# Kernel tuning notes

Hardware: AMD Instinct MI355X
Metric: run time of the kernel (lower is better)

## Reference

```python
import jax, jax.numpy as jnp
import numpy as np

N, E, R = 50000, 500000, 3
IN, HID, OUT = 128, 128, 128
NEG_SLOPE = 0.2


def setup_inputs() -> dict:
    key = jax.random.key(0)
    ks = jax.random.split(key, 16)
    g = lambda i, shape: jax.random.normal(ks[i], shape, jnp.float32) * 0.1
    return {
        "x": jax.random.normal(ks[0], (N, IN), jnp.float32),
        "edge_index": jax.random.randint(ks[1], (2, E), 0, N, jnp.int32),
        "edge_type": jax.random.randint(ks[2], (E,), 0, R, jnp.int32),
        "edge_attr": jax.random.normal(ks[3], (E, 1), jnp.float32),
        # conv1 params (RGATConv: per-relation weight, q/k/e attention vectors, edge lin, bias)
        "w1": g(4, (R, IN, HID)), "q1": g(5, (HID, 1)), "k1": g(6, (HID, 1)),
        "le1": g(7, (1, HID)), "e1": g(8, (HID, 1)), "b1": jnp.zeros((HID,), jnp.float32),
        # conv2 params
        "w2": g(9, (R, HID, OUT)), "q2": g(10, (OUT, 1)), "k2": g(11, (OUT, 1)),
        "le2": g(12, (1, OUT)), "e2": g(13, (OUT, 1)), "b2": jnp.zeros((OUT,), jnp.float32),
    }


def _rgat_conv(x, src, dst, edge_type, edge_attr, w, q, k, le, e, b):
    """PyG RGATConv: heads=1, dim=1, additive-self-attention, across-relation softmax."""
    n = x.shape[0]
    # Per-relation linear at node level (equiv. to per-edge bmm with w[edge_type])
    xw = jnp.einsum('ni,rio->rno', x, w)            # [R, N, C]
    x_j = xw[edge_type, src]                          # [E, C] transformed source feats
    x_i = xw[edge_type, dst]                          # [E, C] transformed target feats
    # additive attention logits: q(x_i) + k(x_j) + e(lin_edge(edge_attr))
    alpha = x_i @ q + x_j @ k + (edge_attr @ le) @ e  # [E, 1]
    alpha = jax.nn.leaky_relu(alpha, negative_slope=NEG_SLOPE)
    # across-relation softmax over incoming edges of each target node
    amax = jax.ops.segment_max(alpha, dst, num_segments=n)
    amax = jnp.where(jnp.isfinite(amax), amax, 0.0)   # empty segments -> 0
    ex = jnp.exp(alpha - amax[dst])
    denom = jax.ops.segment_sum(ex, dst, num_segments=n)
    alpha = ex / (denom[dst] + 1e-16)
    # weighted scatter-add aggregation, then bias (concat=True, heads=1)
    out = jax.ops.segment_sum(alpha * x_j, dst, num_segments=n)  # [N, C]
    return out + b


def reference(x, edge_index, edge_type, edge_attr,
              w1, q1, k1, le1, e1, b1,
              w2, q2, k2, le2, e2, b2):
    src, dst = edge_index[0], edge_index[1]
    h = jax.nn.relu(_rgat_conv(x, src, dst, edge_type, edge_attr, w1, q1, k1, le1, e1, b1))
    return _rgat_conv(h, src, dst, edge_type, edge_attr, w2, q2, k2, le2, e2, b2)
```

## Files before the change

kernel.cpp:

```cpp
#include <hip/hip_runtime.h>
#include <hip/hip_bf16.h>
#include <math.h>

typedef __bf16 bf16x8 __attribute__((ext_vector_type(8)));
typedef float f32x4 __attribute__((ext_vector_type(4)));

#define CDIM 128

__global__ void sentinel_kernel(float* outf) {
  if (threadIdx.x == 0) outf[0] = 12345.0f;
}

__global__ __launch_bounds__(256) void prep_hist_kernel(
    const float* __restrict__ w1, const float* __restrict__ w2,
    __hip_bfloat16* __restrict__ wt,
    const float* __restrict__ le1, const float* __restrict__ e1,
    const float* __restrict__ le2, const float* __restrict__ e2,
    float* __restrict__ outc, const int* __restrict__ dstv,
    int* __restrict__ deg, int perW, int E) {
  const int b = blockIdx.x;
  const int tid = threadIdx.x;
  if (b < 48) {
    int t = b * 256 + tid;
    if (t >= perW * 2) return;
    const float* w = (t < perW) ? w1 : w2;
    int tt = (t < perW) ? t : t - perW;
    int r = tt >> 11;
    int rem = tt & 2047;
    int kb = rem >> 7;
    int o = rem & 127;
    const float* wr = w + ((size_t)r << 14);
    union { __hip_bfloat16 h[8]; int4 v; } u;
#pragma unroll
    for (int j = 0; j < 8; ++j)
      u.h[j] = __float2bfloat16(wr[(size_t)(kb * 8 + j) * CDIM + o]);
    *reinterpret_cast<int4*>(wt + (size_t)t * 8) = u.v;
  } else if (b == 48) {
    if (tid < 64) {
      float v1 = le1[tid] * e1[tid] + le1[tid + 64] * e1[tid + 64];
      float v2 = le2[tid] * e2[tid] + le2[tid + 64] * e2[tid + 64];
#pragma unroll
      for (int off = 32; off > 0; off >>= 1) {
        v1 += __shfl_xor(v1, off, 64);
        v2 += __shfl_xor(v2, off, 64);
      }
      if (tid == 0) { outc[0] = v1; outc[1] = v2; }
    }
  } else {
    int e0 = (b - 49) * 1024 + tid * 4;
    if (e0 + 3 < E) {
      int4 d4 = *reinterpret_cast<const int4*>(&dstv[e0]);
      atomicAdd(&deg[d4.x], 1);
      atomicAdd(&deg[d4.y], 1);
      atomicAdd(&deg[d4.z], 1);
      atomicAdd(&deg[d4.w], 1);
    } else {
      for (int t = 0; t < 4; ++t) {
        int e = e0 + t;
        if (e < E) atomicAdd(&deg[dstv[e]], 1);
      }
    }
  }
}


__global__ __launch_bounds__(256) void scan1_kernel(const int* __restrict__ deg,
                                                    int* __restrict__ rowptr,
                                                    int* __restrict__ partials, int n) {
  __shared__ int sh[256];
  int t = threadIdx.x;
  int base = blockIdx.x * 1024;
  int idx = base + t * 4;
  int v[4]; int s = 0;
#pragma unroll
  for (int j = 0; j < 4; ++j) { v[j] = (idx + j < n) ? deg[idx + j] : 0; s += v[j]; }
  sh[t] = s;
  __syncthreads();
  for (int off = 1; off < 256; off <<= 1) {
    int x = (t >= off) ? sh[t - off] : 0;
    __syncthreads();
    sh[t] += x;
    __syncthreads();
  }
  int excl = sh[t] - s;
  if (t == 255) partials[blockIdx.x] = sh[255];
  int run = excl;
#pragma unroll
  for (int j = 0; j < 4; ++j) {
    if (idx + j < n) rowptr[idx + j] = run;
    run += v[j];
  }
}

__global__ __launch_bounds__(256) void scan3_kernel(int* __restrict__ rowptr,
                                                    int* __restrict__ cursor,
                                                    const int* __restrict__ partials,
                                                    int nb, int n, int E) {
  __shared__ int spfx[64];
  int t = threadIdx.x;
  if (t < 64) {
    int pv = (t < nb) ? partials[t] : 0;
    int v = pv;
#pragma unroll
    for (int off = 1; off < 64; off <<= 1) {
      int u = __shfl_up(v, off, 64);
      if (t >= off) v += u;
    }
    spfx[t] = v - pv;
  }
  __syncthreads();
  int i = blockIdx.x * 256 + t;
  if (i < n) {
    int v = rowptr[i] + spfx[i >> 10];
    rowptr[i] = v;
    cursor[i] = v;
  } else if (i == n) {
    rowptr[n] = E;
  }
}

template <int BF16IN>
__device__ __forceinline__ void gemm_body128(
    int tileb, const float* __restrict__ xf, const __hip_bfloat16* __restrict__ xb,
    const __hip_bfloat16* __restrict__ wt,
    const float* __restrict__ qv, const float* __restrict__ kv,
    __hip_bfloat16* __restrict__ xwout, float* __restrict__ sq,
    float* __restrict__ sk, int n, __hip_bfloat16* wlds, float* qls, float* kls) {
  const int base = tileb * 128;
  const int tid = threadIdx.x;
  const int wave = tid >> 6, lane = tid & 63;
  const int quad = lane >> 4, c16 = lane & 15;

  if (tid < 128) qls[tid] = qv[tid];
  else kls[tid - 128] = kv[tid - 128];

  bf16x8 zf;
#pragma unroll
  for (int j = 0; j < 8; ++j) zf[j] = (__bf16)0.0f;

  bf16x8 af[2][4];
#pragma unroll
  for (int h = 0; h < 2; ++h) {
    int m = base + wave * 32 + h * 16 + c16;
#pragma unroll
    for (int ks = 0; ks < 4; ++ks) {
      if (m < n) {
        if (BF16IN) {
          af[h][ks] = *reinterpret_cast<const bf16x8*>(
              xb + (size_t)m * CDIM + ks * 32 + quad * 8);
        } else {
          const float* xp = xf + (size_t)m * CDIM + ks * 32 + quad * 8;
          f32x4 x0 = *reinterpret_cast<const f32x4*>(xp);
          f32x4 x1 = *reinterpret_cast<const f32x4*>(xp + 4);
          bf16x8 a;
#pragma unroll
          for (int j = 0; j < 4; ++j) { a[j] = (__bf16)x0[j]; a[4 + j] = (__bf16)x1[j]; }
          af[h][ks] = a;
        }
      } else {
        af[h][ks] = zf;
      }
    }
  }

  for (int r = 0; r < 3; ++r) {
    if (r) __syncthreads();
    {
      const int4* src = reinterpret_cast<const int4*>(wt + ((size_t)r << 14));
      int4* dst = reinterpret_cast<int4*>(wlds);
#pragma unroll
      for (int i = 0; i < 8; ++i) dst[tid + i * 256] = src[tid + i * 256];
    }
    __syncthreads();

    f32x4 acc[2][8];
#pragma unroll
    for (int h = 0; h < 2; ++h)
#pragma unroll
      for (int ot = 0; ot < 8; ++ot) acc[h][ot] = (f32x4){0.f, 0.f, 0.f, 0.f};

#pragma unroll
    for (int ks = 0; ks < 4; ++ks) {
#pragma unroll
      for (int ot = 0; ot < 8; ++ot) {
        bf16x8 b = *reinterpret_cast<const bf16x8*>(
            &wlds[(((ks * 4 + quad) * 128) + ot * 16 + c16) * 8]);
        acc[0][ot] = __builtin_amdgcn_mfma_f32_16x16x32_bf16(b, af[0][ks], acc[0][ot], 0, 0, 0);
        acc[1][ot] = __builtin_amdgcn_mfma_f32_16x16x32_bf16(b, af[1][ks], acc[1][ot], 0, 0, 0);
      }
    }

#pragma unroll
    for (int h = 0; h < 2; ++h) {
      const int grow = base + wave * 32 + h * 16 + c16;
      const bool ok = grow < n;
      __hip_bfloat16* rp = xwout + (((size_t)r * n + grow) << 7) + quad * 4;
      float s_q = 0.f, s_k = 0.f;
#pragma unroll
      for (int ot = 0; ot < 8; ++ot) {
        f32x4 a = acc[h][ot];
        f32x4 q4 = *reinterpret_cast<const f32x4*>(&qls[ot * 16 + quad * 4]);
        f32x4 k4 = *reinterpret_cast<const f32x4*>(&kls[ot * 16 + quad * 4]);
        s_q += a[0] * q4[0] + a[1] * q4[1] + a[2] * q4[2] + a[3] * q4[3];
        s_k += a[0] * k4[0] + a[1] * k4[1] + a[2] * k4[2] + a[3] * k4[3];
        if (ok) {
          union { __hip_bfloat16 b4[4]; uint2 u; } pk;
#pragma unroll
          for (int t = 0; t < 4; ++t) pk.b4[t] = __float2bfloat16(a[t]);
          *reinterpret_cast<uint2*>(rp + ot * 16) = pk.u;
        }
      }
      s_q += __shfl_xor(s_q, 16, 64);
      s_q += __shfl_xor(s_q, 32, 64);
      s_k += __shfl_xor(s_k, 16, 64);
      s_k += __shfl_xor(s_k, 32, 64);
      if (quad == 0 && ok) {
        sq[(size_t)r * n + grow] = s_q;
        sk[(size_t)r * n + grow] = s_k;
      }
    }
  }
}

__global__ __launch_bounds__(256) void gemm_scatter_kernel(
    const float* __restrict__ xin, const __hip_bfloat16* __restrict__ wt,
    const float* __restrict__ qv, const float* __restrict__ kv,
    __hip_bfloat16* __restrict__ xwout, float* __restrict__ sq, float* __restrict__ sk,
    const int* __restrict__ srcv, const int* __restrict__ dstv,
    const int* __restrict__ etype, const float* __restrict__ eattr,
    int* __restrict__ cursor, int2* __restrict__ kattr,
    int NT, int n, int E) {
  __shared__ __hip_bfloat16 wlds[16 * 128 * 8];
  __shared__ float qls[128], kls[128];
  const int b = blockIdx.x;
  if (b < NT) {
    gemm_body128<0>(b, xin, nullptr, wt, qv, kv, xwout, sq, sk, n, wlds, qls, kls);
  } else {
    int e0 = (b - NT) * 1024 + threadIdx.x * 4;
    if (e0 + 3 < E) {
      int4 s4 = *reinterpret_cast<const int4*>(&srcv[e0]);
      int4 d4 = *reinterpret_cast<const int4*>(&dstv[e0]);
      int4 t4 = *reinterpret_cast<const int4*>(&etype[e0]);
      float4 a4 = *reinterpret_cast<const float4*>(&eattr[e0]);
      int p0 = atomicAdd(&cursor[d4.x], 1);
      kattr[p0] = make_int2(t4.x * n + s4.x, __float_as_int(a4.x));
      int p1 = atomicAdd(&cursor[d4.y], 1);
      kattr[p1] = make_int2(t4.y * n + s4.y, __float_as_int(a4.y));
      int p2 = atomicAdd(&cursor[d4.z], 1);
      kattr[p2] = make_int2(t4.z * n + s4.z, __float_as_int(a4.z));
      int p3 = atomicAdd(&cursor[d4.w], 1);
      kattr[p3] = make_int2(t4.w * n + s4.w, __float_as_int(a4.w));
    } else {
      for (int t = 0; t < 4; ++t) {
        int e = e0 + t;
        if (e < E) {
          int p = atomicAdd(&cursor[dstv[e]], 1);
          kattr[p] = make_int2(etype[e] * n + srcv[e], __float_as_int(eattr[e]));
        }
      }
    }
  }
}

__global__ __launch_bounds__(256) void gemm_xw_bf16_kernel(
    const __hip_bfloat16* __restrict__ xin, const __hip_bfloat16* __restrict__ wt,
    const float* __restrict__ qv, const float* __restrict__ kv,
    __hip_bfloat16* __restrict__ xwout, float* __restrict__ sq, float* __restrict__ sk,
    int n) {
  __shared__ __hip_bfloat16 wlds[16 * 128 * 8];
  __shared__ float qls[128], kls[128];
  gemm_body128<1>(blockIdx.x, nullptr, xin, wt, qv, kv, xwout, sq, sk, n,
                  wlds, qls, kls);
}

template <int OUTBF16>
__global__ __launch_bounds__(256) void aggregate_kernel(
    const int* __restrict__ rowptr, const int2* __restrict__ kattr,
    const float* __restrict__ sq, const float* __restrict__ sk,
    const __hip_bfloat16* __restrict__ xw, const float* __restrict__ bias,
    const float* __restrict__ cscal, float* __restrict__ outf,
    __hip_bfloat16* __restrict__ outb, int n) {
  const int wave = threadIdx.x >> 6, lane = threadIdx.x & 63;
  const int g = lane >> 4;
  const int sub = lane & 15;
  const int node = blockIdx.x * 16 + wave * 4 + g;
  if (node >= n) return;
  const float c = cscal[0];
  const int n2 = n * 2;

  const int start = rowptr[node];
  const int deg = rowptr[node + 1] - start;
  const float s0 = sq[node], s1 = sq[n + node], s2 = sq[n2 + node];

  float acc[8];
#pragma unroll
  for (int t = 0; t < 8; ++t) acc[t] = 0.f;
  float den = 0.f;

  for (int j0 = 0; j0 < deg; j0 += 4) {
    int2 ka[4];
#pragma unroll
    for (int t = 0; t < 4; ++t) {
      int idx = j0 + t;
      ka[t] = kattr[start + (idx < deg ? idx : 0)];
    }
    float w[4];
    bf16x8 f[4];
#pragma unroll
    for (int t = 0; t < 4; ++t) {
      int kk = ka[t].x;
      float sv = (kk >= n2) ? s2 : ((kk >= n) ? s1 : s0);
      float l = sv + sk[kk] + c * __int_as_float(ka[t].y);
      l = l > 0.f ? l : 0.2f * l;
      w[t] = (j0 + t < deg) ? __expf(l) : 0.f;
      f[t] = *reinterpret_cast<const bf16x8*>(xw + ((size_t)kk << 7) + sub * 8);
    }
#pragma unroll
    for (int t = 0; t < 8; ++t)
      acc[t] += w[0] * (float)f[0][t] + w[1] * (float)f[1][t] +
                w[2] * (float)f[2][t] + w[3] * (float)f[3][t];
    den += (w[0] + w[1]) + (w[2] + w[3]);
  }

  float inv = 1.0f / (den + 1e-16f);
  f32x4 b0 = *reinterpret_cast<const f32x4*>(bias + sub * 8);
  f32x4 b1 = *reinterpret_cast<const f32x4*>(bias + sub * 8 + 4);
  f32x4 o0, o1;
#pragma unroll
  for (int t = 0; t < 4; ++t) {
    o0[t] = acc[t] * inv + b0[t];
    o1[t] = acc[4 + t] * inv + b1[t];
  }
  if (OUTBF16) {
    union { __hip_bfloat16 h[8]; int4 v; } pk;
#pragma unroll
    for (int t = 0; t < 4; ++t) {
      pk.h[t] = __float2bfloat16(fmaxf(o0[t], 0.f));
      pk.h[4 + t] = __float2bfloat16(fmaxf(o1[t], 0.f));
    }
    *reinterpret_cast<int4*>(outb + (size_t)node * CDIM + sub * 8) = pk.v;
  } else {
    float* op = outf + (size_t)node * CDIM + sub * 8;
    *reinterpret_cast<f32x4*>(op) = o0;
    *reinterpret_cast<f32x4*>(op + 4) = o1;
  }
}


extern "C" void kernel_launch(void* const* d_in, const int* in_sizes, int n_in,
                              void* d_out, int out_size, void* d_ws, size_t ws_size,
                              hipStream_t stream) {
  const float* x     = (const float*)d_in[0];
  const int*   eidx  = (const int*)d_in[1];
  const int*   etype = (const int*)d_in[2];
  const float* eattr = (const float*)d_in[3];
  const float* w1  = (const float*)d_in[4];
  const float* q1  = (const float*)d_in[5];
  const float* k1  = (const float*)d_in[6];
  const float* le1 = (const float*)d_in[7];
  const float* e1  = (const float*)d_in[8];
  const float* b1  = (const float*)d_in[9];
  const float* w2  = (const float*)d_in[10];
  const float* q2  = (const float*)d_in[11];
  const float* k2  = (const float*)d_in[12];
  const float* le2 = (const float*)d_in[13];
  const float* e2  = (const float*)d_in[14];
  const float* b2  = (const float*)d_in[15];

  const int N = in_sizes[0] / CDIM;
  const int E = in_sizes[2];
  const int R = in_sizes[4] / (CDIM * CDIM);
  const int* srcv = eidx;
  const int* dstv = eidx + E;

  char* p = (char*)d_ws;
  auto alloc = [&](size_t bytes) -> void* {
    void* q = (void*)p;
    p += (bytes + 255) & ~(size_t)255;
    return q;
  };
  float* sq       = (float*)alloc((size_t)R * N * 4);
  float* sk       = (float*)alloc((size_t)R * N * 4);
  int*   deg      = (int*)alloc((size_t)N * 4);
  int*   rowptr   = (int*)alloc((size_t)(N + 1) * 4);
  int*   cursor   = (int*)alloc((size_t)N * 4);
  int*   partials = (int*)alloc(4096);
  int2*  kattr    = (int2*)alloc((size_t)E * 8);
  __hip_bfloat16* wt = (__hip_bfloat16*)alloc((size_t)2 * R * CDIM * CDIM * 2);
  float* cscal    = (float*)alloc(256);
  __hip_bfloat16* xw = (__hip_bfloat16*)alloc((size_t)R * N * CDIM * 2);
  __hip_bfloat16* hb = (__hip_bfloat16*)alloc((size_t)N * CDIM * 2);

  size_t needed = (size_t)(p - (char*)d_ws);
  if (needed > ws_size) {
    sentinel_kernel<<<1, 64, 0, stream>>>((float*)d_out);
    return;
  }

  float* outp = (float*)d_out;

  const int eg4 = (E + 1023) / 1024;
  const int nb = (N + 1023) / 1024;
  const int NT = (N + 127) / 128;
  const int nodes16 = (N + 15) / 16;
  const int perW = R * 2048;

  hipMemsetAsync(deg, 0, (size_t)N * 4, stream);

  prep_hist_kernel<<<49 + eg4, 256, 0, stream>>>(w1, w2, wt, le1, e1, le2, e2,
                                                 cscal, dstv, deg, perW, E);

  scan1_kernel<<<nb, 256, 0, stream>>>(deg, rowptr, partials, N);
  scan3_kernel<<<(N + 1 + 255) / 256, 256, 0, stream>>>(rowptr, cursor, partials, nb, N, E);

  gemm_scatter_kernel<<<NT + eg4, 256, 0, stream>>>(x, wt, q1, k1, xw, sq, sk,
                                                    srcv, dstv, etype, eattr,
                                                    cursor, kattr, NT, N, E);

  aggregate_kernel<1><<<nodes16, 256, 0, stream>>>(rowptr, kattr, sq, sk, xw, b1,
                                                   cscal + 0, nullptr, hb, N);

  gemm_xw_bf16_kernel<<<NT, 256, 0, stream>>>(hb, wt + (size_t)R * CDIM * CDIM,
                                              q2, k2, xw, sq, sk, N);

  aggregate_kernel<0><<<nodes16, 256, 0, stream>>>(rowptr, kattr, sq, sk, xw, b2,
                                                   cscal + 1, outp, nullptr, N);
}
```

Baseline: 239.8 us.

## Fuse layer-1 aggregation with layer-2 relation GEMM via shared-memory hidden tile

Merges the first aggregation kernel with the second layer's per-relation GEMM. Each block aggregates 64 nodes into a bf16 tile in shared memory and then runs MFMA directly on that tile, so the hidden activation never goes through global memory and one launch is removed. Layer-2 xw, sq and sk now go to separate buffers because other blocks may still be reading layer-1 xw. The trade-offs are that weights are read from global or L2 instead of being staged in LDS, the GEMM tile shrinks to 64 rows, and the workspace grows.

```diff
diff --git a/kernel.cpp b/kernel.cpp
--- a/kernel.cpp
+++ b/kernel.cpp
@@ -119,9 +119,8 @@
   }
 }
 
-template <int BF16IN>
 __device__ __forceinline__ void gemm_body128(
-    int tileb, const float* __restrict__ xf, const __hip_bfloat16* __restrict__ xb,
+    int tileb, const float* __restrict__ xf,
     const __hip_bfloat16* __restrict__ wt,
     const float* __restrict__ qv, const float* __restrict__ kv,
     __hip_bfloat16* __restrict__ xwout, float* __restrict__ sq,
@@ -145,18 +144,13 @@
 #pragma unroll
     for (int ks = 0; ks < 4; ++ks) {
       if (m < n) {
-        if (BF16IN) {
-          af[h][ks] = *reinterpret_cast<const bf16x8*>(
-              xb + (size_t)m * CDIM + ks * 32 + quad * 8);
-        } else {
-          const float* xp = xf + (size_t)m * CDIM + ks * 32 + quad * 8;
-          f32x4 x0 = *reinterpret_cast<const f32x4*>(xp);
-          f32x4 x1 = *reinterpret_cast<const f32x4*>(xp + 4);
-          bf16x8 a;
-#pragma unroll
-          for (int j = 0; j < 4; ++j) { a[j] = (__bf16)x0[j]; a[4 + j] = (__bf16)x1[j]; }
-          af[h][ks] = a;
-        }
+        const float* xp = xf + (size_t)m * CDIM + ks * 32 + quad * 8;
+        f32x4 x0 = *reinterpret_cast<const f32x4*>(xp);
+        f32x4 x1 = *reinterpret_cast<const f32x4*>(xp + 4);
+        bf16x8 a;
+#pragma unroll
+        for (int j = 0; j < 4; ++j) { a[j] = (__bf16)x0[j]; a[4 + j] = (__bf16)x1[j]; }
+        af[h][ks] = a;
       } else {
         af[h][ks] = zf;
       }
@@ -234,7 +228,7 @@
   __shared__ float qls[128], kls[128];
   const int b = blockIdx.x;
   if (b < NT) {
-    gemm_body128<0>(b, xin, nullptr, wt, qv, kv, xwout, sq, sk, n, wlds, qls, kls);
+    gemm_body128(b, xin, wt, qv, kv, xwout, sq, sk, n, wlds, qls, kls);
   } else {
     int e0 = (b - NT) * 1024 + threadIdx.x * 4;
     if (e0 + 3 < E) {
@@ -262,24 +256,138 @@
   }
 }
 
-__global__ __launch_bounds__(256) void gemm_xw_bf16_kernel(
-    const __hip_bfloat16* __restrict__ xin, const __hip_bfloat16* __restrict__ wt,
+__global__ __launch_bounds__(256) void agg_gemm_kernel(
+    const int* __restrict__ rowptr, const int2* __restrict__ kattr,
+    const float* __restrict__ sq1, const float* __restrict__ sk1,
+    const __hip_bfloat16* __restrict__ xw1, const float* __restrict__ bias1,
+    const float* __restrict__ cscal,
+    const __hip_bfloat16* __restrict__ wt2,
     const float* __restrict__ qv, const float* __restrict__ kv,
-    __hip_bfloat16* __restrict__ xwout, float* __restrict__ sq, float* __restrict__ sk,
-    int n) {
-  __shared__ __hip_bfloat16 wlds[16 * 128 * 8];
+    __hip_bfloat16* __restrict__ xw2, float* __restrict__ sq2,
+    float* __restrict__ sk2, int n) {
+  __shared__ __hip_bfloat16 hb[64][144];
   __shared__ float qls[128], kls[128];
-  gemm_body128<1>(blockIdx.x, nullptr, xin, wt, qv, kv, xwout, sq, sk, n,
-                  wlds, qls, kls);
-}
-
-template <int OUTBF16>
+  const int tid = threadIdx.x;
+  const int nodeBase = blockIdx.x * 64;
+  const int grp = tid >> 4, sub = tid & 15;
+  const float c = cscal[0];
+  const int n2 = n * 2;
+
+  if (tid < 128) qls[tid] = qv[tid];
+  else kls[tid - 128] = kv[tid - 128];
+
+#pragma unroll
+  for (int i = 0; i < 4; ++i) {
+    const int lrow = grp * 4 + i;
+    const int node = nodeBase + lrow;
+    if (node < n) {
+      const int start = rowptr[node];
+      const int deg = rowptr[node + 1] - start;
+      const float s0 = sq1[node], s1 = sq1[n + node], s2 = sq1[n2 + node];
+
+      float acc[8];
+#pragma unroll
+      for (int t = 0; t < 8; ++t) acc[t] = 0.f;
+      float den = 0.f;
+
+      for (int j0 = 0; j0 < deg; j0 += 4) {
+        int2 ka[4];
+#pragma unroll
+        for (int t = 0; t < 4; ++t) {
+          int idx = j0 + t;
+          ka[t] = kattr[start + (idx < deg ? idx : 0)];
+        }
+        float w[4];
+        bf16x8 f[4];
+#pragma unroll
+        for (int t = 0; t < 4; ++t) {
+          int kk = ka[t].x;
+          float sv = (kk >= n2) ? s2 : ((kk >= n) ? s1 : s0);
+          float l = sv + sk1[kk] + c * __int_as_float(ka[t].y);
+          l = l > 0.f ? l : 0.2f * l;
+          w[t] = (j0 + t < deg) ? __expf(l) : 0.f;
+          f[t] = *reinterpret_cast<const bf16x8*>(xw1 + ((size_t)kk << 7) + sub * 8);
+        }
+#pragma unroll
+        for (int t = 0; t < 8; ++t)
+          acc[t] += w[0] * (float)f[0][t] + w[1] * (float)f[1][t] +
+                    w[2] * (float)f[2][t] + w[3] * (float)f[3][t];
+        den += (w[0] + w[1]) + (w[2] + w[3]);
+      }
+
+      float inv = 1.0f / (den + 1e-16f);
+      f32x4 b0 = *reinterpret_cast<const f32x4*>(bias1 + sub * 8);
+      f32x4 b1 = *reinterpret_cast<const f32x4*>(bias1 + sub * 8 + 4);
+      union { __hip_bfloat16 h[8]; int4 v; } pk;
+#pragma unroll
+      for (int t = 0; t < 4; ++t) {
+        pk.h[t] = __float2bfloat16(fmaxf(acc[t] * inv + b0[t], 0.f));
+        pk.h[4 + t] = __float2bfloat16(fmaxf(acc[4 + t] * inv + b1[t], 0.f));
+      }
+      *reinterpret_cast<int4*>(&hb[lrow][sub * 8]) = pk.v;
+    }
+  }
+  __syncthreads();
+
+  const int wave = tid >> 6, lane = tid & 63;
+  const int quad = lane >> 4, c16 = lane & 15;
+  const int lrow = wave * 16 + c16;
+  const int m = nodeBase + lrow;
+  const bool ok = m < n;
+
+  bf16x8 af[4];
+#pragma unroll
+  for (int ks = 0; ks < 4; ++ks)
+    af[ks] = *reinterpret_cast<const bf16x8*>(&hb[lrow][ks * 32 + quad * 8]);
+
+  for (int r = 0; r < 3; ++r) {
+    const __hip_bfloat16* wr = wt2 + ((size_t)r << 14);
+    f32x4 acc[8];
+#pragma unroll
+    for (int ot = 0; ot < 8; ++ot) acc[ot] = (f32x4){0.f, 0.f, 0.f, 0.f};
+
+#pragma unroll
+    for (int ks = 0; ks < 4; ++ks) {
+#pragma unroll
+      for (int ot = 0; ot < 8; ++ot) {
+        bf16x8 b = *reinterpret_cast<const bf16x8*>(
+            wr + (size_t)((((ks * 4 + quad) * 128) + ot * 16 + c16) * 8));
+        acc[ot] = __builtin_amdgcn_mfma_f32_16x16x32_bf16(b, af[ks], acc[ot], 0, 0, 0);
+      }
+    }
+
+    __hip_bfloat16* rp = xw2 + (((size_t)r * n + m) << 7) + quad * 4;
+    float s_q = 0.f, s_k = 0.f;
+#pragma unroll
+    for (int ot = 0; ot < 8; ++ot) {
+      f32x4 a = acc[ot];
+      f32x4 q4 = *reinterpret_cast<const f32x4*>(&qls[ot * 16 + quad * 4]);
+      f32x4 k4 = *reinterpret_cast<const f32x4*>(&kls[ot * 16 + quad * 4]);
+      s_q += a[0] * q4[0] + a[1] * q4[1] + a[2] * q4[2] + a[3] * q4[3];
+      s_k += a[0] * k4[0] + a[1] * k4[1] + a[2] * k4[2] + a[3] * k4[3];
+      if (ok) {
+        union { __hip_bfloat16 b4[4]; uint2 u; } pk;
+#pragma unroll
+        for (int t = 0; t < 4; ++t) pk.b4[t] = __float2bfloat16(a[t]);
+        *reinterpret_cast<uint2*>(rp + ot * 16) = pk.u;
+      }
+    }
+    s_q += __shfl_xor(s_q, 16, 64);
+    s_q += __shfl_xor(s_q, 32, 64);
+    s_k += __shfl_xor(s_k, 16, 64);
+    s_k += __shfl_xor(s_k, 32, 64);
+    if (quad == 0 && ok) {
+      sq2[(size_t)r * n + m] = s_q;
+      sk2[(size_t)r * n + m] = s_k;
+    }
+  }
+}
+
 __global__ __launch_bounds__(256) void aggregate_kernel(
     const int* __restrict__ rowptr, const int2* __restrict__ kattr,
     const float* __restrict__ sq, const float* __restrict__ sk,
     const __hip_bfloat16* __restrict__ xw, const float* __restrict__ bias,
-    const float* __restrict__ cscal, float* __restrict__ outf,
-    __hip_bfloat16* __restrict__ outb, int n) {
+    const float* __restrict__ cscal, float* __restrict__ out, int n) {
   const int wave = threadIdx.x >> 6, lane = threadIdx.x & 63;
   const int g = lane >> 4;
   const int sub = lane & 15;
@@ -331,19 +439,9 @@
     o0[t] = acc[t] * inv + b0[t];
     o1[t] = acc[4 + t] * inv + b1[t];
   }
-  if (OUTBF16) {
-    union { __hip_bfloat16 h[8]; int4 v; } pk;
-#pragma unroll
-    for (int t = 0; t < 4; ++t) {
-      pk.h[t] = __float2bfloat16(fmaxf(o0[t], 0.f));
-      pk.h[4 + t] = __float2bfloat16(fmaxf(o1[t], 0.f));
-    }
-    *reinterpret_cast<int4*>(outb + (size_t)node * CDIM + sub * 8) = pk.v;
-  } else {
-    float* op = outf + (size_t)node * CDIM + sub * 8;
-    *reinterpret_cast<f32x4*>(op) = o0;
-    *reinterpret_cast<f32x4*>(op + 4) = o1;
-  }
+  float* op = out + (size_t)node * CDIM + sub * 8;
+  *reinterpret_cast<f32x4*>(op) = o0;
+  *reinterpret_cast<f32x4*>(op + 4) = o1;
 }
 
 
@@ -381,6 +479,8 @@
   };
   float* sq       = (float*)alloc((size_t)R * N * 4);
   float* sk       = (float*)alloc((size_t)R * N * 4);
+  float* sq2      = (float*)alloc((size_t)R * N * 4);
+  float* sk2      = (float*)alloc((size_t)R * N * 4);
   int*   deg      = (int*)alloc((size_t)N * 4);
   int*   rowptr   = (int*)alloc((size_t)(N + 1) * 4);
   int*   cursor   = (int*)alloc((size_t)N * 4);
@@ -388,8 +488,8 @@
   int2*  kattr    = (int2*)alloc((size_t)E * 8);
   __hip_bfloat16* wt = (__hip_bfloat16*)alloc((size_t)2 * R * CDIM * CDIM * 2);
   float* cscal    = (float*)alloc(256);
-  __hip_bfloat16* xw = (__hip_bfloat16*)alloc((size_t)R * N * CDIM * 2);
-  __hip_bfloat16* hb = (__hip_bfloat16*)alloc((size_t)N * CDIM * 2);
+  __hip_bfloat16* xw  = (__hip_bfloat16*)alloc((size_t)R * N * CDIM * 2);
+  __hip_bfloat16* xw2 = (__hip_bfloat16*)alloc((size_t)R * N * CDIM * 2);
 
   size_t needed = (size_t)(p - (char*)d_ws);
   if (needed > ws_size) {
@@ -402,6 +502,7 @@
   const int eg4 = (E + 1023) / 1024;
   const int nb = (N + 1023) / 1024;
   const int NT = (N + 127) / 128;
+  const int NG = (N + 63) / 64;
   const int nodes16 = (N + 15) / 16;
   const int perW = R * 2048;
 
@@ -417,12 +518,10 @@
                                                     srcv, dstv, etype, eattr,
                                                     cursor, kattr, NT, N, E);
 
-  aggregate_kernel<1><<<nodes16, 256, 0, stream>>>(rowptr, kattr, sq, sk, xw, b1,
-                                                   cscal + 0, nullptr, hb, N);
-
-  gemm_xw_bf16_kernel<<<NT, 256, 0, stream>>>(hb, wt + (size_t)R * CDIM * CDIM,
-                                              q2, k2, xw, sq, sk, N);
-
-  aggregate_kernel<0><<<nodes16, 256, 0, stream>>>(rowptr, kattr, sq, sk, xw, b2,
-                                                   cscal + 1, outp, nullptr, N);
-}
+  agg_gemm_kernel<<<NG, 256, 0, stream>>>(rowptr, kattr, sq, sk, xw, b1,
+                                          cscal + 0, wt + (size_t)R * CDIM * CDIM,
+                                          q2, k2, xw2, sq2, sk2, N);
+
+  aggregate_kernel<<<nodes16, 256, 0, stream>>>(rowptr, kattr, sq2, sk2, xw2, b2,
+                                                cscal + 1, outp, N);
+}
```

Result: slower. 264.1 us (+10.1%).
